# Kernel optimization log

Hardware: AMD Instinct MI355X
Metric: run time of the kernel (lower is better)

## Reference

```python
import jax, jax.numpy as jnp
import numpy as np

N = 100000
E = 3200000
IN_C = 128
HID = 16
OUT_C = 16
EA = 16


def setup_inputs() -> dict:
    key = jax.random.key(0)
    ks = jax.random.split(key, 8)
    x = jax.random.normal(ks[0], (N, IN_C), dtype=jnp.float32)
    edge_index = jax.random.randint(ks[1], (2, E), 0, N, dtype=jnp.int32)
    edge_attr = jax.random.normal(ks[2], (E, EA), dtype=jnp.float32)
    We = jax.random.normal(ks[3], (EA, HID), dtype=jnp.float32) * (1.0 / np.sqrt(EA))
    be = jnp.zeros((HID,), dtype=jnp.float32)
    W1 = jax.random.normal(ks[4], (IN_C, HID), dtype=jnp.float32) * (1.0 / np.sqrt(IN_C))
    b1 = jnp.zeros((HID,), dtype=jnp.float32)
    W2 = jax.random.normal(ks[5], (HID, OUT_C), dtype=jnp.float32) * (1.0 / np.sqrt(HID))
    b2 = jnp.zeros((OUT_C,), dtype=jnp.float32)
    return {"x": x, "edge_index": edge_index, "edge_attr": edge_attr,
            "We": We, "be": be, "W1": W1, "b1": b1, "W2": W2, "b2": b2}


def _gcn_conv(h, src, dst, ew, dinv_src, dinv_dst, dinv_sq, W, b):
    # h: [N, Cin] -> transform first (PyG order), then normalized gather-scatter.
    h = h @ W                                   # [N, C], C == HID == OUT_C == 16
    norm = dinv_src * ew * dinv_dst             # [E, 16] per-edge per-channel norm
    msg = norm * h[src]                          # gather + fuse edge weight
    agg = jax.ops.segment_sum(msg, dst, num_segments=N)  # scatter-add
    agg = agg + dinv_sq * h                      # self-loop (weight 1) contribution
    return agg + b


def reference(x, edge_index, edge_attr, We, be, W1, b1, W2, b2):
    src, dst = edge_index[0], edge_index[1]
    ew = edge_attr @ We + be                     # [E, 16] edge weights (per channel)
    # symmetric degree normalization with self loops (weight 1), per channel
    deg = jax.ops.segment_sum(ew, dst, num_segments=N) + 1.0  # [N, 16]
    dinv = jnp.where(deg > 0, jax.lax.rsqrt(jnp.abs(deg) + 1e-12), 0.0)
    dinv_src = dinv[src]
    dinv_dst = dinv[dst]
    dinv_sq = dinv * dinv
    h = jax.nn.relu(_gcn_conv(x, src, dst, ew, dinv_src, dinv_dst, dinv_sq, W1, b1))
    # dropout is identity in eval mode
    out = _gcn_conv(h, src, dst, ew, dinv_src, dinv_dst, dinv_sq, W2, b2)
    return out
```

## Files before the change

kernel.cpp:

```cpp
#include <hip/hip_runtime.h>

static constexpr int N_NODES = 100000;
static constexpr int N_EDGES = 3200000;
static constexpr int NC16    = N_NODES * 16;
static constexpr int RB      = 64;
static constexpr int NB      = (N_NODES + RB - 1) / RB;
static constexpr int CAP     = 2560;
static constexpr int NPB     = 512;
static constexpr int EPB     = N_EDGES / NPB;

__device__ __forceinline__ float4 v4fma(float s, float4 w, float4 acc) {
    acc.x = fmaf(s, w.x, acc.x);
    acc.y = fmaf(s, w.y, acc.y);
    acc.z = fmaf(s, w.z, acc.z);
    acc.w = fmaf(s, w.w, acc.w);
    return acc;
}

template<int KK>
__device__ __forceinline__ float4 qbcast(float4 a) {
    constexpr int ctrl = KK * 0x55;
    float4 r;
    r.x = __int_as_float(__builtin_amdgcn_mov_dpp(__float_as_int(a.x), ctrl, 0xF, 0xF, true));
    r.y = __int_as_float(__builtin_amdgcn_mov_dpp(__float_as_int(a.y), ctrl, 0xF, 0xF, true));
    r.z = __int_as_float(__builtin_amdgcn_mov_dpp(__float_as_int(a.z), ctrl, 0xF, 0xF, true));
    r.w = __int_as_float(__builtin_amdgcn_mov_dpp(__float_as_int(a.w), ctrl, 0xF, 0xF, true));
    return r;
}

template<int KK>
__device__ __forceinline__ float4 ewstep(float4 a, const float4* wc, float4 ew) {
    float4 v = qbcast<KK>(a);
    ew = v4fma(v.x, wc[4*KK + 0], ew);
    ew = v4fma(v.y, wc[4*KK + 1], ew);
    ew = v4fma(v.z, wc[4*KK + 2], ew);
    ew = v4fma(v.w, wc[4*KK + 3], ew);
    return ew;
}

__device__ __forceinline__ void accum4(double* __restrict__ accS, int dl, int c4,
                                       double v0, double v1, double v2, double v3) {
    double* row = accS + dl * 16;
    const int pb = (c4 * 4 + dl) & 15;
    atomicAdd(row + ((pb + 0) & 15), v0);
    atomicAdd(row + ((pb + 1) & 15), v1);
    atomicAdd(row + ((pb + 2) & 15), v2);
    atomicAdd(row + ((pb + 3) & 15), v3);
}

__global__ __launch_bounds__(256)
void k_zero(int* g) {
    int t = blockIdx.x * 256 + threadIdx.x;
    if (t < NB) g[t] = 0;
}

__global__ __launch_bounds__(1024)
void k_part(const int* __restrict__ srcI, const int* __restrict__ dstI,
            int* __restrict__ gcount, int2* __restrict__ meta)
{
    __shared__ int hist[NB];
    const int tid = threadIdx.x;
    const int e0  = blockIdx.x * EPB;
    for (int t = tid; t < NB; t += 1024) hist[t] = 0;
    __syncthreads();
    for (int i = tid; i < EPB; i += 1024) {
        int d = dstI[e0 + i];
        atomicAdd(&hist[d >> 6], 1);
    }
    __syncthreads();
    for (int t = tid; t < NB; t += 1024) {
        int h = hist[t];
        hist[t] = (h > 0) ? atomicAdd(&gcount[t], h) : 0;
    }
    __syncthreads();
    for (int i = tid; i < EPB; i += 1024) {
        int e = e0 + i;
        int d = dstI[e];
        int s = srcI[e];
        int b = d >> 6;
        int pos = atomicAdd(&hist[b], 1);
        if (pos < CAP)
            meta[b * CAP + pos] = make_int2(e, (s << 6) | (d & 63));
    }
}

__global__ __launch_bounds__(512)
void k_deg(const float* __restrict__ ea, const int2* __restrict__ meta,
           const int* __restrict__ gcount, const float* __restrict__ We,
           const float* __restrict__ be,
           const float* __restrict__ x, const float* __restrict__ W1,
           float* __restrict__ dinv, float* __restrict__ pA)
{
    __shared__ double accS[RB * 16];
    __shared__ float4 w1s[512];
    const int tid = threadIdx.x;
    const int b   = blockIdx.x;
    for (int t = tid; t < RB * 16; t += 512) accS[t] = 0.0;
    w1s[tid] = ((const float4*)W1)[tid];

    const int c4 = tid & 3;
    float4 wc[16];
    const float4* We4 = (const float4*)We;
#pragma unroll
    for (int k = 0; k < 16; ++k) wc[k] = We4[k * 4 + c4];
    const float4 bev = ((const float4*)be)[c4];
    const int cnt = min(gcount[b], CAP);
    const int2* ml = meta + b * CAP;
    const float4* ea4 = (const float4*)ea;
    __syncthreads();

#pragma unroll 2
    for (int i = tid >> 2; i < cnt; i += 128) {
        int2 m = ml[i];
        float4 a = ea4[m.x * 4 + c4];
        const int dl = m.y & 63;
        float4 ew = bev;
        ew = ewstep<0>(a, wc, ew);
        ew = ewstep<1>(a, wc, ew);
        ew = ewstep<2>(a, wc, ew);
        ew = ewstep<3>(a, wc, ew);
        accum4(accS, dl, c4, (double)ew.x, (double)ew.y, (double)ew.z, (double)ew.w);
    }
    __syncthreads();

    if (tid < RB * 4) {
        const int nl = tid >> 2;
        const int ng = b * RB + nl;
        if (ng < N_NODES) {
            const double* s = accS + nl * 16;
            const int pb = (c4 * 4 + nl) & 15;
            float4 dv;
            float d0 = (float)s[(pb + 0) & 15] + 1.0f; dv.x = (d0 > 0.f) ? rsqrtf(d0 + 1e-12f) : 0.f;
            float d1 = (float)s[(pb + 1) & 15] + 1.0f; dv.y = (d1 > 0.f) ? rsqrtf(d1 + 1e-12f) : 0.f;
            float d2 = (float)s[(pb + 2) & 15] + 1.0f; dv.z = (d2 > 0.f) ? rsqrtf(d2 + 1e-12f) : 0.f;
            float d3 = (float)s[(pb + 3) & 15] + 1.0f; dv.w = (d3 > 0.f) ? rsqrtf(d3 + 1e-12f) : 0.f;
            ((float4*)dinv)[ng * 4 + c4] = dv;

            const float4* x4 = (const float4*)x;
            float4 acc = make_float4(0.f, 0.f, 0.f, 0.f);
            for (int k4 = 0; k4 < 32; ++k4) {
                float4 xv = x4[ng * 32 + k4];
                acc = v4fma(xv.x, w1s[(k4 * 4 + 0) * 4 + c4], acc);
                acc = v4fma(xv.y, w1s[(k4 * 4 + 1) * 4 + c4], acc);
                acc = v4fma(xv.z, w1s[(k4 * 4 + 2) * 4 + c4], acc);
                acc = v4fma(xv.w, w1s[(k4 * 4 + 3) * 4 + c4], acc);
            }
            float4 o;
            o.x = dv.x * acc.x; o.y = dv.y * acc.y;
            o.z = dv.z * acc.z; o.w = dv.w * acc.w;
            ((float4*)pA)[ng * 4 + c4] = o;
        }
    }
}

template<int FIN>
__global__ __launch_bounds__(512)
void k_gather(const float* __restrict__ ea, const int2* __restrict__ meta,
              const int* __restrict__ gcount, const float* __restrict__ We,
              const float* __restrict__ be, const float* __restrict__ dinv,
              const float* __restrict__ pin, const float* __restrict__ Wb,
              const float* __restrict__ b1, float* __restrict__ pout)
{
    __shared__ double accS[RB * 16];
    const int tid = threadIdx.x;
    const int b   = blockIdx.x;
    for (int t = tid; t < RB * 16; t += 512) accS[t] = 0.0;

    const int c4 = tid & 3;
    float4 wc[16];
    const float4* We4 = (const float4*)We;
#pragma unroll
    for (int k = 0; k < 16; ++k) wc[k] = We4[k * 4 + c4];
    const float4 bev = ((const float4*)be)[c4];
    const int cnt = min(gcount[b], CAP);
    const int2* ml = meta + b * CAP;
    const float4* ea4 = (const float4*)ea;
    const float4* p4  = (const float4*)pin;
    __syncthreads();

#pragma unroll 2
    for (int i = tid >> 2; i < cnt; i += 128) {
        int2 m = ml[i];
        float4 a = ea4[m.x * 4 + c4];
        float4 pv = p4[((unsigned)m.y >> 6) * 4 + c4];
        const int dl = m.y & 63;
        float4 ew = bev;
        ew = ewstep<0>(a, wc, ew);
        ew = ewstep<1>(a, wc, ew);
        ew = ewstep<2>(a, wc, ew);
        ew = ewstep<3>(a, wc, ew);
        accum4(accS, dl, c4,
               (double)(ew.x * pv.x), (double)(ew.y * pv.y),
               (double)(ew.z * pv.z), (double)(ew.w * pv.w));
    }
    __syncthreads();

    if (tid < RB * 4) {
        const int nl = tid >> 2;
        const int ng = b * RB + nl;
        if (ng < N_NODES) {
            const double* s = accS + nl * 16;
            const int pb = (c4 * 4 + nl) & 15;
            float4 av;
            av.x = (float)s[(pb + 0) & 15];
            av.y = (float)s[(pb + 1) & 15];
            av.z = (float)s[(pb + 2) & 15];
            av.w = (float)s[(pb + 3) & 15];
            const float4 pv = ((const float4*)pin)[ng * 4 + c4];
            const float4 dv = ((const float4*)dinv)[ng * 4 + c4];
            float4 o;
            if (FIN == 0) {
                const float4 b1v = ((const float4*)b1)[c4];
                float4 h1;
                h1.x = fmaxf(fmaf(dv.x, av.x + pv.x, b1v.x), 0.f);
                h1.y = fmaxf(fmaf(dv.y, av.y + pv.y, b1v.y), 0.f);
                h1.z = fmaxf(fmaf(dv.z, av.z + pv.z, b1v.z), 0.f);
                h1.w = fmaxf(fmaf(dv.w, av.w + pv.w, b1v.w), 0.f);
                float4 wc2[16];
                const float4* W24 = (const float4*)Wb;
#pragma unroll
                for (int k = 0; k < 16; ++k) wc2[k] = W24[k * 4 + c4];
                float4 h2 = make_float4(0.f, 0.f, 0.f, 0.f);
                h2 = ewstep<0>(h1, wc2, h2);
                h2 = ewstep<1>(h1, wc2, h2);
                h2 = ewstep<2>(h1, wc2, h2);
                h2 = ewstep<3>(h1, wc2, h2);
                o.x = dv.x * h2.x; o.y = dv.y * h2.y;
                o.z = dv.z * h2.z; o.w = dv.w * h2.w;
            } else {
                const float4 b2v = ((const float4*)Wb)[c4];
                o.x = fmaf(dv.x, av.x + pv.x, b2v.x);
                o.y = fmaf(dv.y, av.y + pv.y, b2v.y);
                o.z = fmaf(dv.z, av.z + pv.z, b2v.z);
                o.w = fmaf(dv.w, av.w + pv.w, b2v.w);
            }
            ((float4*)pout)[ng * 4 + c4] = o;
        }
    }
}

extern "C" void kernel_launch(void* const* d_in, const int* in_sizes, int n_in,
                              void* d_out, int out_size, void* d_ws, size_t ws_size,
                              hipStream_t stream)
{
    const float* x   = (const float*)d_in[0];
    const int*   ei  = (const int*)d_in[1];
    const float* ea  = (const float*)d_in[2];
    const float* We  = (const float*)d_in[3];
    const float* be  = (const float*)d_in[4];
    const float* W1  = (const float*)d_in[5];
    const float* b1  = (const float*)d_in[6];
    const float* W2  = (const float*)d_in[7];
    const float* b2  = (const float*)d_in[8];
    float* out = (float*)d_out;

    const int* srcI = ei;
    const int* dstI = ei + N_EDGES;

    float* dinv = (float*)d_ws;
    float* pA   = dinv + NC16;
    float* pB   = pA + NC16;
    int2*  meta = (int2*)(pB + NC16);
    int*   gcount = (int*)(meta + (size_t)NB * CAP);

    hipLaunchKernelGGL(k_zero, dim3((NB + 255) / 256), dim3(256), 0, stream, gcount);
    hipLaunchKernelGGL(k_part, dim3(NPB), dim3(1024), 0, stream,
                       srcI, dstI, gcount, meta);
    hipLaunchKernelGGL(k_deg, dim3(NB), dim3(512), 0, stream,
                       ea, meta, gcount, We, be, x, W1, dinv, pA);
    hipLaunchKernelGGL((k_gather<0>), dim3(NB), dim3(512), 0, stream,
                       ea, meta, gcount, We, be, dinv, pA, W2, b1, pB);
    hipLaunchKernelGGL((k_gather<1>), dim3(NB), dim3(512), 0, stream,
                       ea, meta, gcount, We, be, dinv, pB, b2, (const float*)nullptr, out);
}
```

Baseline: 685.4 us.

## Sort bucket edges by local destination in LDS and accumulate runs in registers

Merges the degree and gather kernels into one templated edge kernel. Each block counting-sorts its bucket's edge metadata by local destination node into shared memory. Each quad of threads then walks a contiguous slice and accumulates runs of edges with the same destination in registers, flushing to the shared double accumulators only when the destination changes. This cuts the number of shared-memory atomic/double accumulations, at the cost of an extra sort pass with atomics, about 20KB more LDS per block, and likely uneven slice lengths across threads.

```diff
diff --git a/kernel.cpp b/kernel.cpp
--- a/kernel.cpp
+++ b/kernel.cpp
@@ -84,19 +84,46 @@
     }
 }
 
+template<int MODE>
 __global__ __launch_bounds__(512)
-void k_deg(const float* __restrict__ ea, const int2* __restrict__ meta,
-           const int* __restrict__ gcount, const float* __restrict__ We,
-           const float* __restrict__ be,
-           const float* __restrict__ x, const float* __restrict__ W1,
-           float* __restrict__ dinv, float* __restrict__ pA)
+void k_edge(const float* __restrict__ ea, const int2* __restrict__ meta,
+            const int* __restrict__ gcount, const float* __restrict__ We,
+            const float* __restrict__ be,
+            const float* __restrict__ x, const float* __restrict__ W1,
+            float* __restrict__ dinv, const float* __restrict__ pin,
+            const float* __restrict__ Wb, const float* __restrict__ b1,
+            float* __restrict__ pout)
 {
     __shared__ double accS[RB * 16];
-    __shared__ float4 w1s[512];
+    __shared__ int2  metaS[CAP];
+    __shared__ int   hist[RB];
+    __shared__ int   basep[RB];
+    __shared__ int   curs[RB];
+    __shared__ float4 w1s[(MODE == 0) ? 512 : 4];
     const int tid = threadIdx.x;
     const int b   = blockIdx.x;
     for (int t = tid; t < RB * 16; t += 512) accS[t] = 0.0;
-    w1s[tid] = ((const float4*)W1)[tid];
+    if (tid < RB) { hist[tid] = 0; curs[tid] = 0; }
+    if (MODE == 0) w1s[tid] = ((const float4*)W1)[tid];
+
+    const int cnt = min(gcount[b], CAP);
+    const int2* mlG = meta + b * CAP;
+    __syncthreads();
+
+    for (int i = tid; i < cnt; i += 512)
+        atomicAdd(&hist[mlG[i].y & 63], 1);
+    __syncthreads();
+    if (tid == 0) {
+        int s = 0;
+        for (int k = 0; k < RB; ++k) { basep[k] = s; s += hist[k]; }
+    }
+    __syncthreads();
+    for (int i = tid; i < cnt; i += 512) {
+        int2 m = mlG[i];
+        int dl = m.y & 63;
+        int pos = basep[dl] + atomicAdd(&curs[dl], 1);
+        metaS[pos] = m;
+    }
 
     const int c4 = tid & 3;
     float4 wc[16];
@@ -104,22 +131,39 @@
 #pragma unroll
     for (int k = 0; k < 16; ++k) wc[k] = We4[k * 4 + c4];
     const float4 bev = ((const float4*)be)[c4];
-    const int cnt = min(gcount[b], CAP);
-    const int2* ml = meta + b * CAP;
     const float4* ea4 = (const float4*)ea;
-    __syncthreads();
-
+    const float4* p4  = (const float4*)pin;
+    __syncthreads();
+
+    {
+        const int q  = tid >> 2;
+        const int L  = (cnt + 127) >> 7;
+        const int j0 = q * L;
+        const int j1 = min(j0 + L, cnt);
+        double r0 = 0.0, r1 = 0.0, r2 = 0.0, r3 = 0.0;
+        int rdl = -1;
 #pragma unroll 2
-    for (int i = tid >> 2; i < cnt; i += 128) {
-        int2 m = ml[i];
-        float4 a = ea4[m.x * 4 + c4];
-        const int dl = m.y & 63;
-        float4 ew = bev;
-        ew = ewstep<0>(a, wc, ew);
-        ew = ewstep<1>(a, wc, ew);
-        ew = ewstep<2>(a, wc, ew);
-        ew = ewstep<3>(a, wc, ew);
-        accum4(accS, dl, c4, (double)ew.x, (double)ew.y, (double)ew.z, (double)ew.w);
+        for (int j = j0; j < j1; ++j) {
+            int2 m = metaS[j];
+            float4 a = ea4[m.x * 4 + c4];
+            float4 ew = bev;
+            ew = ewstep<0>(a, wc, ew);
+            ew = ewstep<1>(a, wc, ew);
+            ew = ewstep<2>(a, wc, ew);
+            ew = ewstep<3>(a, wc, ew);
+            if (MODE != 0) {
+                float4 pv = p4[((unsigned)m.y >> 6) * 4 + c4];
+                ew.x *= pv.x; ew.y *= pv.y; ew.z *= pv.z; ew.w *= pv.w;
+            }
+            int dl = m.y & 63;
+            if (dl != rdl) {
+                if (rdl >= 0) accum4(accS, rdl, c4, r0, r1, r2, r3);
+                rdl = dl; r0 = r1 = r2 = r3 = 0.0;
+            }
+            r0 += (double)ew.x; r1 += (double)ew.y;
+            r2 += (double)ew.z; r3 += (double)ew.w;
+        }
+        if (rdl >= 0) accum4(accS, rdl, c4, r0, r1, r2, r3);
     }
     __syncthreads();
 
@@ -129,112 +173,62 @@
         if (ng < N_NODES) {
             const double* s = accS + nl * 16;
             const int pb = (c4 * 4 + nl) & 15;
-            float4 dv;
-            float d0 = (float)s[(pb + 0) & 15] + 1.0f; dv.x = (d0 > 0.f) ? rsqrtf(d0 + 1e-12f) : 0.f;
-            float d1 = (float)s[(pb + 1) & 15] + 1.0f; dv.y = (d1 > 0.f) ? rsqrtf(d1 + 1e-12f) : 0.f;
-            float d2 = (float)s[(pb + 2) & 15] + 1.0f; dv.z = (d2 > 0.f) ? rsqrtf(d2 + 1e-12f) : 0.f;
-            float d3 = (float)s[(pb + 3) & 15] + 1.0f; dv.w = (d3 > 0.f) ? rsqrtf(d3 + 1e-12f) : 0.f;
-            ((float4*)dinv)[ng * 4 + c4] = dv;
-
-            const float4* x4 = (const float4*)x;
-            float4 acc = make_float4(0.f, 0.f, 0.f, 0.f);
-            for (int k4 = 0; k4 < 32; ++k4) {
-                float4 xv = x4[ng * 32 + k4];
-                acc = v4fma(xv.x, w1s[(k4 * 4 + 0) * 4 + c4], acc);
-                acc = v4fma(xv.y, w1s[(k4 * 4 + 1) * 4 + c4], acc);
-                acc = v4fma(xv.z, w1s[(k4 * 4 + 2) * 4 + c4], acc);
-                acc = v4fma(xv.w, w1s[(k4 * 4 + 3) * 4 + c4], acc);
+            if (MODE == 0) {
+                float4 dv;
+                float d0 = (float)s[(pb + 0) & 15] + 1.0f; dv.x = (d0 > 0.f) ? rsqrtf(d0 + 1e-12f) : 0.f;
+                float d1 = (float)s[(pb + 1) & 15] + 1.0f; dv.y = (d1 > 0.f) ? rsqrtf(d1 + 1e-12f) : 0.f;
+                float d2 = (float)s[(pb + 2) & 15] + 1.0f; dv.z = (d2 > 0.f) ? rsqrtf(d2 + 1e-12f) : 0.f;
+                float d3 = (float)s[(pb + 3) & 15] + 1.0f; dv.w = (d3 > 0.f) ? rsqrtf(d3 + 1e-12f) : 0.f;
+                ((float4*)dinv)[ng * 4 + c4] = dv;
+                const float4* x4 = (const float4*)x;
+                float4 acc = make_float4(0.f, 0.f, 0.f, 0.f);
+                for (int k4 = 0; k4 < 32; ++k4) {
+                    float4 xv = x4[ng * 32 + k4];
+                    acc = v4fma(xv.x, w1s[(k4 * 4 + 0) * 4 + c4], acc);
+                    acc = v4fma(xv.y, w1s[(k4 * 4 + 1) * 4 + c4], acc);
+                    acc = v4fma(xv.z, w1s[(k4 * 4 + 2) * 4 + c4], acc);
+                    acc = v4fma(xv.w, w1s[(k4 * 4 + 3) * 4 + c4], acc);
+                }
+                float4 o;
+                o.x = dv.x * acc.x; o.y = dv.y * acc.y;
+                o.z = dv.z * acc.z; o.w = dv.w * acc.w;
+                ((float4*)pout)[ng * 4 + c4] = o;
+            } else {
+                float4 av;
+                av.x = (float)s[(pb + 0) & 15];
+                av.y = (float)s[(pb + 1) & 15];
+                av.z = (float)s[(pb + 2) & 15];
+                av.w = (float)s[(pb + 3) & 15];
+                const float4 pv = ((const float4*)pin)[ng * 4 + c4];
+                const float4 dv = ((const float4*)dinv)[ng * 4 + c4];
+                float4 o;
+                if (MODE == 1) {
+                    const float4 b1v = ((const float4*)b1)[c4];
+                    float4 h1;
+                    h1.x = fmaxf(fmaf(dv.x, av.x + pv.x, b1v.x), 0.f);
+                    h1.y = fmaxf(fmaf(dv.y, av.y + pv.y, b1v.y), 0.f);
+                    h1.z = fmaxf(fmaf(dv.z, av.z + pv.z, b1v.z), 0.f);
+                    h1.w = fmaxf(fmaf(dv.w, av.w + pv.w, b1v.w), 0.f);
+                    float4 wc2[16];
+                    const float4* W24 = (const float4*)Wb;
+#pragma unroll
+                    for (int k = 0; k < 16; ++k) wc2[k] = W24[k * 4 + c4];
+                    float4 h2 = make_float4(0.f, 0.f, 0.f, 0.f);
+                    h2 = ewstep<0>(h1, wc2, h2);
+                    h2 = ewstep<1>(h1, wc2, h2);
+                    h2 = ewstep<2>(h1, wc2, h2);
+                    h2 = ewstep<3>(h1, wc2, h2);
+                    o.x = dv.x * h2.x; o.y = dv.y * h2.y;
+                    o.z = dv.z * h2.z; o.w = dv.w * h2.w;
+                } else {
+                    const float4 b2v = ((const float4*)Wb)[c4];
+                    o.x = fmaf(dv.x, av.x + pv.x, b2v.x);
+                    o.y = fmaf(dv.y, av.y + pv.y, b2v.y);
+                    o.z = fmaf(dv.z, av.z + pv.z, b2v.z);
+                    o.w = fmaf(dv.w, av.w + pv.w, b2v.w);
+                }
+                ((float4*)pout)[ng * 4 + c4] = o;
             }
-            float4 o;
-            o.x = dv.x * acc.x; o.y = dv.y * acc.y;
-            o.z = dv.z * acc.z; o.w = dv.w * acc.w;
-            ((float4*)pA)[ng * 4 + c4] = o;
-        }
-    }
-}
-
-template<int FIN>
-__global__ __launch_bounds__(512)
-void k_gather(const float* __restrict__ ea, const int2* __restrict__ meta,
-              const int* __restrict__ gcount, const float* __restrict__ We,
-              const float* __restrict__ be, const float* __restrict__ dinv,
-              const float* __restrict__ pin, const float* __restrict__ Wb,
-              const float* __restrict__ b1, float* __restrict__ pout)
-{
-    __shared__ double accS[RB * 16];
-    const int tid = threadIdx.x;
-    const int b   = blockIdx.x;
-    for (int t = tid; t < RB * 16; t += 512) accS[t] = 0.0;
-
-    const int c4 = tid & 3;
-    float4 wc[16];
-    const float4* We4 = (const float4*)We;
-#pragma unroll
-    for (int k = 0; k < 16; ++k) wc[k] = We4[k * 4 + c4];
-    const float4 bev = ((const float4*)be)[c4];
-    const int cnt = min(gcount[b], CAP);
-    const int2* ml = meta + b * CAP;
-    const float4* ea4 = (const float4*)ea;
-    const float4* p4  = (const float4*)pin;
-    __syncthreads();
-
-#pragma unroll 2
-    for (int i = tid >> 2; i < cnt; i += 128) {
-        int2 m = ml[i];
-        float4 a = ea4[m.x * 4 + c4];
-        float4 pv = p4[((unsigned)m.y >> 6) * 4 + c4];
-        const int dl = m.y & 63;
-        float4 ew = bev;
-        ew = ewstep<0>(a, wc, ew);
-        ew = ewstep<1>(a, wc, ew);
-        ew = ewstep<2>(a, wc, ew);
-        ew = ewstep<3>(a, wc, ew);
-        accum4(accS, dl, c4,
-               (double)(ew.x * pv.x), (double)(ew.y * pv.y),
-               (double)(ew.z * pv.z), (double)(ew.w * pv.w));
-    }
-    __syncthreads();
-
-    if (tid < RB * 4) {
-        const int nl = tid >> 2;
-        const int ng = b * RB + nl;
-        if (ng < N_NODES) {
-            const double* s = accS + nl * 16;
-            const int pb = (c4 * 4 + nl) & 15;
-            float4 av;
-            av.x = (float)s[(pb + 0) & 15];
-            av.y = (float)s[(pb + 1) & 15];
-            av.z = (float)s[(pb + 2) & 15];
-            av.w = (float)s[(pb + 3) & 15];
-            const float4 pv = ((const float4*)pin)[ng * 4 + c4];
-            const float4 dv = ((const float4*)dinv)[ng * 4 + c4];
-            float4 o;
-            if (FIN == 0) {
-                const float4 b1v = ((const float4*)b1)[c4];
-                float4 h1;
-                h1.x = fmaxf(fmaf(dv.x, av.x + pv.x, b1v.x), 0.f);
-                h1.y = fmaxf(fmaf(dv.y, av.y + pv.y, b1v.y), 0.f);
-                h1.z = fmaxf(fmaf(dv.z, av.z + pv.z, b1v.z), 0.f);
-                h1.w = fmaxf(fmaf(dv.w, av.w + pv.w, b1v.w), 0.f);
-                float4 wc2[16];
-                const float4* W24 = (const float4*)Wb;
-#pragma unroll
-                for (int k = 0; k < 16; ++k) wc2[k] = W24[k * 4 + c4];
-                float4 h2 = make_float4(0.f, 0.f, 0.f, 0.f);
-                h2 = ewstep<0>(h1, wc2, h2);
-                h2 = ewstep<1>(h1, wc2, h2);
-                h2 = ewstep<2>(h1, wc2, h2);
-                h2 = ewstep<3>(h1, wc2, h2);
-                o.x = dv.x * h2.x; o.y = dv.y * h2.y;
-                o.z = dv.z * h2.z; o.w = dv.w * h2.w;
-            } else {
-                const float4 b2v = ((const float4*)Wb)[c4];
-                o.x = fmaf(dv.x, av.x + pv.x, b2v.x);
-                o.y = fmaf(dv.y, av.y + pv.y, b2v.y);
-                o.z = fmaf(dv.z, av.z + pv.z, b2v.z);
-                o.w = fmaf(dv.w, av.w + pv.w, b2v.w);
-            }
-            ((float4*)pout)[ng * 4 + c4] = o;
         }
     }
 }
@@ -266,10 +260,15 @@
     hipLaunchKernelGGL(k_zero, dim3((NB + 255) / 256), dim3(256), 0, stream, gcount);
     hipLaunchKernelGGL(k_part, dim3(NPB), dim3(1024), 0, stream,
                        srcI, dstI, gcount, meta);
-    hipLaunchKernelGGL(k_deg, dim3(NB), dim3(512), 0, stream,
-                       ea, meta, gcount, We, be, x, W1, dinv, pA);
-    hipLaunchKernelGGL((k_gather<0>), dim3(NB), dim3(512), 0, stream,
-                       ea, meta, gcount, We, be, dinv, pA, W2, b1, pB);
-    hipLaunchKernelGGL((k_gather<1>), dim3(NB), dim3(512), 0, stream,
-                       ea, meta, gcount, We, be, dinv, pB, b2, (const float*)nullptr, out);
-}
+    hipLaunchKernelGGL((k_edge<0>), dim3(NB), dim3(512), 0, stream,
+                       ea, meta, gcount, We, be, x, W1, dinv,
+                       (const float*)nullptr, (const float*)nullptr,
+                       (const float*)nullptr, pA);
+    hipLaunchKernelGGL((k_edge<1>), dim3(NB), dim3(512), 0, stream,
+                       ea, meta, gcount, We, be, (const float*)nullptr,
+                       (const float*)nullptr, dinv, pA, W2, b1, pB);
+    hipLaunchKernelGGL((k_edge<2>), dim3(NB), dim3(512), 0, stream,
+                       ea, meta, gcount, We, be, (const float*)nullptr,
+                       (const float*)nullptr, dinv, pB, b2,
+                       (const float*)nullptr, out);
+}
```

Result: no change. 690.1 us (+0.7%).
